# Optimization experiments

Hardware: AMD Instinct MI355X
Metric: run time of the kernel (lower is better)

## Reference

```python
import jax, jax.numpy as jnp
import numpy as np

N = 50000
E = 800000
IN_C = 256
OUT_C = 128
HID = 2 * OUT_C  # 256


def setup_inputs() -> dict:
    key = jax.random.key(0)
    ks = jax.random.split(key, 8)
    def glorot(k, fan_in, fan_out):
        lim = (6.0 / (fan_in + fan_out)) ** 0.5
        return jax.random.uniform(k, (fan_in, fan_out), jnp.float32, -lim, lim)
    x = jax.random.normal(ks[0], (N, IN_C), dtype=jnp.float32)
    edge_index = jax.random.randint(ks[1], (2, E), 0, N, dtype=jnp.int64)
    return {
        "x": x,
        "edge_index": edge_index,
        "W1": glorot(ks[2], IN_C, HID),
        "b1": jnp.zeros((HID,), jnp.float32),
        "W_mu": glorot(ks[3], HID, OUT_C),
        "b_mu": jnp.zeros((OUT_C,), jnp.float32),
        "W_ls": glorot(ks[4], HID, OUT_C),
        "b_ls": jnp.zeros((OUT_C,), jnp.float32),
    }


def _gcn_norm(edge_index, n):
    # PyG GCNConv default: add self-loops, symmetric normalization D^-1/2 A D^-1/2
    loop = jnp.arange(n, dtype=edge_index.dtype)
    src = jnp.concatenate([edge_index[0], loop])  # [E+N]
    dst = jnp.concatenate([edge_index[1], loop])
    deg = jax.ops.segment_sum(jnp.ones_like(dst, dtype=jnp.float32), dst, num_segments=n)
    dinv = jnp.where(deg > 0, jax.lax.rsqrt(deg), 0.0)
    norm = dinv[src] * dinv[dst]  # [E+N]
    return src, dst, norm


def _gcn_conv(x, W, b, src, dst, norm, n):
    h = x @ W                                   # [N, F_out] transform first (F_out < F_in ok)
    msg = h[src] * norm[:, None]                # [E+N, F_out] gather + scale
    out = jax.ops.segment_sum(msg, dst, num_segments=n)  # scatter-add aggregate
    return out + b


def reference(x, edge_index, W1, b1, W_mu, b_mu, W_ls, b_ls):
    n = x.shape[0]
    src, dst, norm = _gcn_norm(edge_index, n)
    h = jax.nn.relu(_gcn_conv(x, W1, b1, src, dst, norm, n))
    mu = _gcn_conv(h, W_mu, b_mu, src, dst, norm, n)
    logstd = _gcn_conv(h, W_ls, b_ls, src, dst, norm, n)
    return (mu, logstd)
```

## Files before the change

### kernel.cpp

```cpp
#include <hip/hip_runtime.h>

#define NN 50000
#define EE 800000
#define NBIN 391
#define BINCAP 2560
#define NB_P1 391
#define NB_PB 256

typedef _Float16 half8 __attribute__((ext_vector_type(8)));
typedef float f32x4 __attribute__((ext_vector_type(4)));
typedef unsigned short ushort8v __attribute__((ext_vector_type(8)));
typedef unsigned short ushort4v __attribute__((ext_vector_type(4)));

__device__ __forceinline__ unsigned short f2h(float f){
  _Float16 h = (_Float16)f; unsigned short u; __builtin_memcpy(&u, &h, 2); return u;
}
__device__ __forceinline__ float h2f(unsigned short u){
  _Float16 h; __builtin_memcpy(&h, &u, 2); return (float)h;
}
__device__ __forceinline__ void split2h(float v, unsigned short* p){
  _Float16 hi = (_Float16)v;
  _Float16 lo = (_Float16)(v - (float)hi);
  __builtin_memcpy(p, &hi, 2);
  __builtin_memcpy(p+1, &lo, 2);
}
__device__ __forceinline__ void gl2lds16(const unsigned short* g, unsigned short* l){
  __builtin_amdgcn_global_load_lds(
    (const __attribute__((address_space(1))) unsigned int*)g,
    (__attribute__((address_space(3))) unsigned int*)l, 16, 0, 0);
}

__device__ __forceinline__ int detect_m(const int* eidx, int* sh){
  int t = threadIdx.x;
  if (t < 64){
    int v = eidx[2*t + 1];
    unsigned long long nz = __ballot(v != 0);
    if (t == 0) *sh = (nz == 0ULL) ? 1 : 0;
  }
  __syncthreads();
  return *sh;
}

__global__ __launch_bounds__(512) void k_prep(const int* __restrict__ eidx,
    const float* __restrict__ W1,
    const float* __restrict__ Wmu, const float* __restrict__ Wls,
    int* __restrict__ gcur, unsigned int* __restrict__ binbuf,
    unsigned short* __restrict__ Bt1, unsigned short* __restrict__ Bt2){
  int b = blockIdx.x;
  int tid = threadIdx.x;
  if (b < NB_P1){
    __shared__ int msh;
    __shared__ int hist[NBIN];
    __shared__ int base[NBIN];
    int m = detect_m(eidx, &msh);
    for (int k = tid; k < NBIN; k += 512) hist[k] = 0;
    __syncthreads();
    int sv[4], dl[4], cb[4], ofs[4];
    #pragma unroll
    for (int j = 0; j < 4; ++j){
      int e = b*2048 + j*512 + tid;
      cb[j] = -1;
      if (e < EE){
        sv[j] = m ? eidx[2*e]        : eidx[e];
        int d  = m ? eidx[2*(EE + e)] : eidx[EE + e];
        cb[j] = d >> 7; dl[j] = d & 127;
        ofs[j] = atomicAdd(&hist[cb[j]], 1);
      }
    }
    __syncthreads();
    for (int k = tid; k < NBIN; k += 512)
      base[k] = hist[k] ? atomicAdd(&gcur[k], hist[k]) : 0;
    __syncthreads();
    #pragma unroll
    for (int j = 0; j < 4; ++j){
      if (cb[j] >= 0){
        int p = base[cb[j]] + ofs[j];
        if (p < BINCAP)
          binbuf[(size_t)cb[j]*BINCAP + p] = (unsigned)sv[j] | ((unsigned)dl[j] << 16);
      }
    }
  } else {
    int gid = (b - NB_P1)*512 + tid;
    int idx = gid & 65535;
    int n = idx & 255, k = idx >> 8;
    if (gid < 65536){
      unsigned short hq = f2h(W1[k*256 + n]);
      unsigned short* p = Bt1 + (size_t)n*512 + 2*k;
      p[0] = hq; p[1] = hq;
    } else {
      float w = (n < 128) ? Wmu[k*128 + n] : Wls[k*128 + (n - 128)];
      Bt2[(size_t)n*256 + k] = f2h(w);
    }
  }
}

__global__ __launch_bounds__(512) void k_pass2(const unsigned int* __restrict__ binbuf,
    const int* __restrict__ gcur, int* __restrict__ cnt,
    unsigned short* __restrict__ bk){
  __shared__ int lcnt[128];
  __shared__ __align__(16) unsigned short lbk[128*64];
  int c = blockIdx.x;
  int tid = threadIdx.x;
  if (tid < 128) lcnt[tid] = 0;
  __syncthreads();
  int n = gcur[c]; if (n > BINCAP) n = BINCAP;
  const unsigned int* bb = binbuf + (size_t)c*BINCAP;
  for (int t = tid; t < n; t += 512){
    unsigned v = bb[t];
    int dloc = v >> 16;
    int slot = atomicAdd(&lcnt[dloc], 1);
    if (slot < 64) lbk[dloc*64 + slot] = (unsigned short)(v & 0xFFFF);
  }
  __syncthreads();
  #pragma unroll
  for (int k = 0; k < 2; ++k){
    int idx = k*512 + tid;
    int node = c*128 + (idx >> 3);
    if (node < NN)
      *(uint4*)(bk + (size_t)c*128*64 + idx*8) = *(const uint4*)(lbk + idx*8);
  }
  if (tid < 128){
    int node = c*128 + tid;
    if (node < NN) cnt[node] = lcnt[tid];
  }
}

__global__ __launch_bounds__(256) void k_gemm8x(const float* __restrict__ X,
    const unsigned short* __restrict__ Bt, unsigned short* __restrict__ C,
    int M, const int* __restrict__ cnt){
  __shared__ __align__(16) unsigned short sA[128*64];
  __shared__ __align__(16) unsigned short sB[128*64];
  const int g = blockIdx.x;
  const int xc = g & 7, s = g >> 3;
  const int tN = s & 1;
  const int tM = (s >> 1)*8 + xc;
  const int nTM = (M + 127) >> 7;
  if (tM >= nTM) return;
  const int tid  = threadIdx.x;
  const int wave = tid >> 6, lane = tid & 63;
  const int wm = wave >> 1, wn = wave & 1;
  const int quad = lane >> 4, l16 = lane & 15;
  const int rsub = lane >> 3;
  const int l7   = lane & 7;
  const int chs  = l7 ^ rsub;

  f32x4 acc[4][4] = {};

  for (int kt = 0; kt < 8; ++kt){
    #pragma unroll
    for (int j = 0; j < 4; ++j){
      int q = wave*4 + j;
      int r = q*8 + rsub;
      gl2lds16(Bt + (size_t)(tN*128 + r)*512 + kt*64 + chs*8, &sB[q*512]);
    }
    float4 v[4];
    #pragma unroll
    for (int j = 0; j < 4; ++j){
      int q = wave*4 + j;
      int r = q*8 + rsub;
      int arow = tM*128 + r; if (arow >= M) arow = M-1;
      v[j] = *(const float4*)(X + (size_t)arow*256 + kt*32 + chs*4);
    }
    #pragma unroll
    for (int j = 0; j < 4; ++j){
      int q = wave*4 + j;
      __attribute__((aligned(16))) unsigned short sh[8];
      split2h(v[j].x, sh); split2h(v[j].y, sh+2);
      split2h(v[j].z, sh+4); split2h(v[j].w, sh+6);
      *(uint4*)(&sA[q*512 + (rsub*8 + l7)*8]) = *(const uint4*)(sh);
    }
    __syncthreads();
    #pragma unroll
    for (int ks = 0; ks < 2; ++ks){
      half8 af[4], bfr[4];
      #pragma unroll
      for (int t = 0; t < 4; ++t){
        int R = wm*64 + t*16 + l16;
        af[t]  = *(const half8*)(&sA[R*64 + ((ks*4 + quad) ^ (R & 7))*8]);
      }
      #pragma unroll
      for (int t = 0; t < 4; ++t){
        int R = wn*64 + t*16 + l16;
        bfr[t] = *(const half8*)(&sB[R*64 + ((ks*4 + quad) ^ (R & 7))*8]);
      }
      #pragma unroll
      for (int mt = 0; mt < 4; ++mt)
        #pragma unroll
        for (int nt = 0; nt < 4; ++nt)
          acc[mt][nt] = __builtin_amdgcn_mfma_f32_16x16x32_f16(af[mt], bfr[nt], acc[mt][nt], 0, 0, 0);
    }
    __syncthreads();
  }

  #pragma unroll
  for (int mt = 0; mt < 4; ++mt){
    #pragma unroll
    for (int r = 0; r < 4; ++r){
      int row = tM*128 + wm*64 + mt*16 + quad*4 + r;
      if (row < M){
        float sc = rsqrtf((float)(cnt[row] + 1));
        #pragma unroll
        for (int nt = 0; nt < 4; ++nt){
          int cc = tN*128 + wn*64 + nt*16 + l16;
          C[(size_t)row*256 + cc] = f2h(acc[mt][nt][r] * sc);
        }
      }
    }
  }
}

template<int KT, int SCALE>
__global__ __launch_bounds__(256) void k_gemm(const unsigned short* __restrict__ Asp,
                                              const unsigned short* __restrict__ Bt,
                                              unsigned short* __restrict__ C, int M,
                                              const int* __restrict__ cnt){
  __shared__ __align__(16) unsigned short sA[128*64];
  __shared__ __align__(16) unsigned short sB[128*64];
  const int g = blockIdx.x;
  const int xc = g & 7, s = g >> 3;
  const int tN = s & 1;
  const int tM = (s >> 1)*8 + xc;
  const int nTM = (M + 127) >> 7;
  if (tM >= nTM) return;
  const int tid  = threadIdx.x;
  const int wave = tid >> 6, lane = tid & 63;
  const int wm = wave >> 1, wn = wave & 1;
  const int quad = lane >> 4, l16 = lane & 15;
  const int rsub = lane >> 3;
  const int chs  = (lane & 7) ^ rsub;

  f32x4 acc[4][4] = {};

  for (int kt = 0; kt < KT; ++kt){
    #pragma unroll
    for (int j = 0; j < 4; ++j){
      int q = wave*4 + j;
      int r = q*8 + rsub;
      int arow = tM*128 + r; if (arow >= M) arow = M-1;
      gl2lds16(Asp + (size_t)arow*(KT*64) + kt*64 + chs*8, &sA[q*512]);
      gl2lds16(Bt  + (size_t)(tN*128 + r)*(KT*64) + kt*64 + chs*8, &sB[q*512]);
    }
    __syncthreads();
    #pragma unroll
    for (int ks = 0; ks < 2; ++ks){
      half8 af[4], bfr[4];
      #pragma unroll
      for (int t = 0; t < 4; ++t){
        int R = wm*64 + t*16 + l16;
        af[t]  = *(const half8*)(&sA[R*64 + ((ks*4 + quad) ^ (R & 7))*8]);
      }
      #pragma unroll
      for (int t = 0; t < 4; ++t){
        int R = wn*64 + t*16 + l16;
        bfr[t] = *(const half8*)(&sB[R*64 + ((ks*4 + quad) ^ (R & 7))*8]);
      }
      #pragma unroll
      for (int mt = 0; mt < 4; ++mt)
        #pragma unroll
        for (int nt = 0; nt < 4; ++nt)
          acc[mt][nt] = __builtin_amdgcn_mfma_f32_16x16x32_f16(af[mt], bfr[nt], acc[mt][nt], 0, 0, 0);
    }
    __syncthreads();
  }

  #pragma unroll
  for (int mt = 0; mt < 4; ++mt){
    #pragma unroll
    for (int r = 0; r < 4; ++r){
      int row = tM*128 + wm*64 + mt*16 + quad*4 + r;
      if (row < M){
        float sc = 1.f;
        if (SCALE) sc = rsqrtf((float)(cnt[row] + 1));
        #pragma unroll
        for (int nt = 0; nt < 4; ++nt){
          int cc = tN*128 + wn*64 + nt*16 + l16;
          C[(size_t)row*256 + cc] = f2h(acc[mt][nt][r] * sc);
        }
      }
    }
  }
}

__global__ __launch_bounds__(256) void k_agg_relu(const unsigned short* __restrict__ feat,
    const int* __restrict__ cnt, const unsigned short* __restrict__ bkall,
    const float* __restrict__ b1, unsigned short* __restrict__ h1){
  int i = blockIdx.x*4 + (threadIdx.x >> 6);
  int lane = threadIdx.x & 63;
  int f0 = lane*4;
  int deg = cnt[i]; if (deg > 64) deg = 64;
  float di = rsqrtf((float)(deg + 1));
  const unsigned short* bk = bkall + ((size_t)i << 6);
  ushort4 hv = *(const ushort4*)(feat + (size_t)i*256 + f0);
  float p0 = h2f(hv.x), p1 = h2f(hv.y), p2 = h2f(hv.z), p3 = h2f(hv.w);
  float q0=0.f,q1=0.f,q2=0.f,q3=0.f, r0=0.f,r1=0.f,r2=0.f,r3=0.f, t0=0.f,t1=0.f,t2=0.f,t3=0.f;
  int e = 0;
  for (; e + 8 <= deg; e += 8){
    ushort8v sa = *(const ushort8v*)(bk + e);
    ushort4 v0 = *(const ushort4*)(feat + (size_t)sa[0]*256 + f0);
    ushort4 v1 = *(const ushort4*)(feat + (size_t)sa[1]*256 + f0);
    ushort4 v2 = *(const ushort4*)(feat + (size_t)sa[2]*256 + f0);
    ushort4 v3 = *(const ushort4*)(feat + (size_t)sa[3]*256 + f0);
    ushort4 v4 = *(const ushort4*)(feat + (size_t)sa[4]*256 + f0);
    ushort4 v5 = *(const ushort4*)(feat + (size_t)sa[5]*256 + f0);
    ushort4 v6 = *(const ushort4*)(feat + (size_t)sa[6]*256 + f0);
    ushort4 v7 = *(const ushort4*)(feat + (size_t)sa[7]*256 + f0);
    p0 += h2f(v0.x); p1 += h2f(v0.y); p2 += h2f(v0.z); p3 += h2f(v0.w);
    q0 += h2f(v1.x); q1 += h2f(v1.y); q2 += h2f(v1.z); q3 += h2f(v1.w);
    r0 += h2f(v2.x); r1 += h2f(v2.y); r2 += h2f(v2.z); r3 += h2f(v2.w);
    t0 += h2f(v3.x); t1 += h2f(v3.y); t2 += h2f(v3.z); t3 += h2f(v3.w);
    p0 += h2f(v4.x); p1 += h2f(v4.y); p2 += h2f(v4.z); p3 += h2f(v4.w);
    q0 += h2f(v5.x); q1 += h2f(v5.y); q2 += h2f(v5.z); q3 += h2f(v5.w);
    r0 += h2f(v6.x); r1 += h2f(v6.y); r2 += h2f(v6.z); r3 += h2f(v6.w);
    t0 += h2f(v7.x); t1 += h2f(v7.y); t2 += h2f(v7.z); t3 += h2f(v7.w);
  }
  if (e + 4 <= deg){
    ushort4v sa = *(const ushort4v*)(bk + e);
    ushort4 v0 = *(const ushort4*)(feat + (size_t)sa[0]*256 + f0);
    ushort4 v1 = *(const ushort4*)(feat + (size_t)sa[1]*256 + f0);
    ushort4 v2 = *(const ushort4*)(feat + (size_t)sa[2]*256 + f0);
    ushort4 v3 = *(const ushort4*)(feat + (size_t)sa[3]*256 + f0);
    p0 += h2f(v0.x); p1 += h2f(v0.y); p2 += h2f(v0.z); p3 += h2f(v0.w);
    q0 += h2f(v1.x); q1 += h2f(v1.y); q2 += h2f(v1.z); q3 += h2f(v1.w);
    r0 += h2f(v2.x); r1 += h2f(v2.y); r2 += h2f(v2.z); r3 += h2f(v2.w);
    t0 += h2f(v3.x); t1 += h2f(v3.y); t2 += h2f(v3.z); t3 += h2f(v3.w);
    e += 4;
  }
  for (; e < deg; ++e){
    int s = bk[e];
    ushort4 v = *(const ushort4*)(feat + (size_t)s*256 + f0);
    p0 += h2f(v.x); p1 += h2f(v.y); p2 += h2f(v.z); p3 += h2f(v.w);
  }
  float s0 = p0+q0+r0+t0, s1 = p1+q1+r1+t1, s2 = p2+q2+r2+t2, s3 = p3+q3+r3+t3;
  float4 bb = *(const float4*)(b1 + f0);
  float u0 = fmaxf(di*s0 + bb.x, 0.f);
  float u1 = fmaxf(di*s1 + bb.y, 0.f);
  float u2 = fmaxf(di*s2 + bb.z, 0.f);
  float u3 = fmaxf(di*s3 + bb.w, 0.f);
  ushort4 o;
  o.x = f2h(di*u0); o.y = f2h(di*u1); o.z = f2h(di*u2); o.w = f2h(di*u3);
  *(ushort4*)(h1 + (size_t)i*256 + f0) = o;
}

__global__ __launch_bounds__(256) void k_agg_out(const unsigned short* __restrict__ feat,
    const int* __restrict__ cnt, const unsigned short* __restrict__ bkall,
    const float* __restrict__ bmu, const float* __restrict__ bls, float* __restrict__ outp){
  int i = blockIdx.x*4 + (threadIdx.x >> 6);
  int lane = threadIdx.x & 63;
  int f0 = lane*4;
  int deg = cnt[i]; if (deg > 64) deg = 64;
  float di = rsqrtf((float)(deg + 1));
  const unsigned short* bk = bkall + ((size_t)i << 6);
  ushort4 hv = *(const ushort4*)(feat + (size_t)i*256 + f0);
  float p0 = h2f(hv.x), p1 = h2f(hv.y), p2 = h2f(hv.z), p3 = h2f(hv.w);
  float q0=0.f,q1=0.f,q2=0.f,q3=0.f, r0=0.f,r1=0.f,r2=0.f,r3=0.f, t0=0.f,t1=0.f,t2=0.f,t3=0.f;
  int e = 0;
  for (; e + 8 <= deg; e += 8){
    ushort8v sa = *(const ushort8v*)(bk + e);
    ushort4 v0 = *(const ushort4*)(feat + (size_t)sa[0]*256 + f0);
    ushort4 v1 = *(const ushort4*)(feat + (size_t)sa[1]*256 + f0);
    ushort4 v2 = *(const ushort4*)(feat + (size_t)sa[2]*256 + f0);
    ushort4 v3 = *(const ushort4*)(feat + (size_t)sa[3]*256 + f0);
    ushort4 v4 = *(const ushort4*)(feat + (size_t)sa[4]*256 + f0);
    ushort4 v5 = *(const ushort4*)(feat + (size_t)sa[5]*256 + f0);
    ushort4 v6 = *(const ushort4*)(feat + (size_t)sa[6]*256 + f0);
    ushort4 v7 = *(const ushort4*)(feat + (size_t)sa[7]*256 + f0);
    p0 += h2f(v0.x); p1 += h2f(v0.y); p2 += h2f(v0.z); p3 += h2f(v0.w);
    q0 += h2f(v1.x); q1 += h2f(v1.y); q2 += h2f(v1.z); q3 += h2f(v1.w);
    r0 += h2f(v2.x); r1 += h2f(v2.y); r2 += h2f(v2.z); r3 += h2f(v2.w);
    t0 += h2f(v3.x); t1 += h2f(v3.y); t2 += h2f(v3.z); t3 += h2f(v3.w);
    p0 += h2f(v4.x); p1 += h2f(v4.y); p2 += h2f(v4.z); p3 += h2f(v4.w);
    q0 += h2f(v5.x); q1 += h2f(v5.y); q2 += h2f(v5.z); q3 += h2f(v5.w);
    r0 += h2f(v6.x); r1 += h2f(v6.y); r2 += h2f(v6.z); r3 += h2f(v6.w);
    t0 += h2f(v7.x); t1 += h2f(v7.y); t2 += h2f(v7.z); t3 += h2f(v7.w);
  }
  if (e + 4 <= deg){
    ushort4v sa = *(const ushort4v*)(bk + e);
    ushort4 v0 = *(const ushort4*)(feat + (size_t)sa[0]*256 + f0);
    ushort4 v1 = *(const ushort4*)(feat + (size_t)sa[1]*256 + f0);
    ushort4 v2 = *(const ushort4*)(feat + (size_t)sa[2]*256 + f0);
    ushort4 v3 = *(const ushort4*)(feat + (size_t)sa[3]*256 + f0);
    p0 += h2f(v0.x); p1 += h2f(v0.y); p2 += h2f(v0.z); p3 += h2f(v0.w);
    q0 += h2f(v1.x); q1 += h2f(v1.y); q2 += h2f(v1.z); q3 += h2f(v1.w);
    r0 += h2f(v2.x); r1 += h2f(v2.y); r2 += h2f(v2.z); r3 += h2f(v2.w);
    t0 += h2f(v3.x); t1 += h2f(v3.y); t2 += h2f(v3.z); t3 += h2f(v3.w);
    e += 4;
  }
  for (; e < deg; ++e){
    int s = bk[e];
    ushort4 v = *(const ushort4*)(feat + (size_t)s*256 + f0);
    p0 += h2f(v.x); p1 += h2f(v.y); p2 += h2f(v.z); p3 += h2f(v.w);
  }
  float a0 = di*(p0+q0+r0+t0), a1 = di*(p1+q1+r1+t1);
  float a2 = di*(p2+q2+r2+t2), a3 = di*(p3+q3+r3+t3);
  float4 o;
  if (f0 < 128){
    float4 bb = *(const float4*)(bmu + f0);
    o.x = a0 + bb.x; o.y = a1 + bb.y; o.z = a2 + bb.z; o.w = a3 + bb.w;
    *(float4*)(outp + (size_t)i*128 + f0) = o;
  } else {
    int g = f0 - 128;
    float4 bb = *(const float4*)(bls + g);
    o.x = a0 + bb.x; o.y = a1 + bb.y; o.z = a2 + bb.z; o.w = a3 + bb.w;
    *(float4*)(outp + (size_t)NN*128 + (size_t)i*128 + g) = o;
  }
}

extern "C" void kernel_launch(void* const* d_in, const int* in_sizes, int n_in,
                              void* d_out, int out_size, void* d_ws, size_t ws_size,
                              hipStream_t stream){
  const float* x   = (const float*)d_in[0];
  const int* eidx  = (const int*)d_in[1];
  const float* W1  = (const float*)d_in[2];
  const float* b1  = (const float*)d_in[3];
  const float* Wmu = (const float*)d_in[4];
  const float* bmu = (const float*)d_in[5];
  const float* Wls = (const float*)d_in[6];
  const float* bls = (const float*)d_in[7];
  float* out = (float*)d_out;

  char* ws = (char*)d_ws;
  size_t off = 0;
  auto alloc = [&](size_t bytes)->char*{
    char* p = ws + off; off = (off + bytes + 511) & ~(size_t)511; return p;
  };
  int* gcur     = (int*)alloc(NBIN*4);
  unsigned int* binbuf = (unsigned int*)alloc((size_t)NBIN*BINCAP*4);
  int* cnt      = (int*)alloc(NN*4);
  unsigned short* buckets = (unsigned short*)alloc((size_t)NN*64*2);
  unsigned short* Bt1 = (unsigned short*)alloc((size_t)256*512*2);
  unsigned short* Bt2 = (unsigned short*)alloc((size_t)256*256*2);
  unsigned short* h1  = (unsigned short*)alloc((size_t)NN*256*2);
  unsigned short* h   = (unsigned short*)alloc((size_t)NN*256*2);
  unsigned short* z   = h;

  hipMemsetAsync(gcur, 0, NBIN*4, stream);
  k_prep<<<NB_P1 + NB_PB, 512, 0, stream>>>(eidx, W1, Wmu, Wls,
                                            gcur, binbuf, Bt1, Bt2);
  k_pass2<<<NBIN, 512, 0, stream>>>(binbuf, gcur, cnt, buckets);
  k_gemm8x<<<784, 256, 0, stream>>>(x, Bt1, h, NN, cnt);
  k_agg_relu<<<12500, 256, 0, stream>>>(h, cnt, buckets, b1, h1);
  k_gemm<4,0><<<784, 256, 0, stream>>>(h1, Bt2, z, NN, cnt);
  k_agg_out<<<12500, 256, 0, stream>>>(z, cnt, buckets, bmu, bls, out);
}
```

Before: 294.8 us.

## Software-pipeline both GEMM kernels with double-buffered B tiles and register-prefetched A

Both GEMM kernels now double-buffer the B tile in LDS and prefetch the next A slice into registers while the current K-step's MFMAs run, using explicit waitcnt and s_barrier in place of __syncthreads. The second GEMM loads A through registers instead of direct global-to-LDS copies, and its unused scale path is dropped. Launch bounds request 3 blocks per CU. The aim is to hide global load latency behind compute, at the cost of more LDS and registers per block, which could limit occupancy.

```diff
diff --git a/kernel.cpp b/kernel.cpp
--- a/kernel.cpp
+++ b/kernel.cpp
@@ -125,11 +125,11 @@
   }
 }
 
-__global__ __launch_bounds__(256) void k_gemm8x(const float* __restrict__ X,
+__global__ __launch_bounds__(256, 3) void k_gemm8x(const float* __restrict__ X,
     const unsigned short* __restrict__ Bt, unsigned short* __restrict__ C,
     int M, const int* __restrict__ cnt){
   __shared__ __align__(16) unsigned short sA[128*64];
-  __shared__ __align__(16) unsigned short sB[128*64];
+  __shared__ __align__(16) unsigned short sB[2][128*64];
   const int g = blockIdx.x;
   const int xc = g & 7, s = g >> 3;
   const int tN = s & 1;
@@ -144,32 +144,53 @@
   const int l7   = lane & 7;
   const int chs  = l7 ^ rsub;
 
+  int arow[4];
+  #pragma unroll
+  for (int j = 0; j < 4; ++j){
+    int q = wave*4 + j, r = q*8 + rsub;
+    int a = tM*128 + r; if (a >= M) a = M-1;
+    arow[j] = a;
+  }
+
   f32x4 acc[4][4] = {};
 
+  #pragma unroll
+  for (int j = 0; j < 4; ++j){
+    int q = wave*4 + j, r = q*8 + rsub;
+    gl2lds16(Bt + (size_t)(tN*128 + r)*512 + chs*8, &sB[0][q*512]);
+  }
+  __builtin_amdgcn_sched_barrier(0);
+  float4 v[4];
+  float4 vn[4] = {};
+  #pragma unroll
+  for (int j = 0; j < 4; ++j)
+    v[j] = *(const float4*)(X + (size_t)arow[j]*256 + chs*4);
+
+  #pragma unroll
   for (int kt = 0; kt < 8; ++kt){
-    #pragma unroll
-    for (int j = 0; j < 4; ++j){
-      int q = wave*4 + j;
-      int r = q*8 + rsub;
-      gl2lds16(Bt + (size_t)(tN*128 + r)*512 + kt*64 + chs*8, &sB[q*512]);
-    }
-    float4 v[4];
-    #pragma unroll
-    for (int j = 0; j < 4; ++j){
-      int q = wave*4 + j;
-      int r = q*8 + rsub;
-      int arow = tM*128 + r; if (arow >= M) arow = M-1;
-      v[j] = *(const float4*)(X + (size_t)arow*256 + kt*32 + chs*4);
-    }
     #pragma unroll
     for (int j = 0; j < 4; ++j){
       int q = wave*4 + j;
       __attribute__((aligned(16))) unsigned short sh[8];
-      split2h(v[j].x, sh); split2h(v[j].y, sh+2);
+      split2h(v[j].x, sh);   split2h(v[j].y, sh+2);
       split2h(v[j].z, sh+4); split2h(v[j].w, sh+6);
-      *(uint4*)(&sA[q*512 + (rsub*8 + l7)*8]) = *(const uint4*)(sh);
-    }
-    __syncthreads();
+      *(uint4*)(&sA[q*512 + lane*8]) = *(const uint4*)(sh);
+    }
+    if (kt < 7){
+      #pragma unroll
+      for (int j = 0; j < 4; ++j){
+        int q = wave*4 + j, r = q*8 + rsub;
+        gl2lds16(Bt + (size_t)(tN*128 + r)*512 + (kt+1)*64 + chs*8,
+                 &sB[(kt+1)&1][q*512]);
+      }
+      __builtin_amdgcn_sched_barrier(0);
+      #pragma unroll
+      for (int j = 0; j < 4; ++j)
+        vn[j] = *(const float4*)(X + (size_t)arow[j]*256 + (kt+1)*32 + chs*4);
+    }
+    asm volatile("s_waitcnt lgkmcnt(0)" ::: "memory");
+    __builtin_amdgcn_sched_barrier(0);
+    __builtin_amdgcn_s_barrier();
     #pragma unroll
     for (int ks = 0; ks < 2; ++ks){
       half8 af[4], bfr[4];
@@ -181,7 +202,7 @@
       #pragma unroll
       for (int t = 0; t < 4; ++t){
         int R = wn*64 + t*16 + l16;
-        bfr[t] = *(const half8*)(&sB[R*64 + ((ks*4 + quad) ^ (R & 7))*8]);
+        bfr[t] = *(const half8*)(&sB[kt & 1][R*64 + ((ks*4 + quad) ^ (R & 7))*8]);
       }
       #pragma unroll
       for (int mt = 0; mt < 4; ++mt)
@@ -189,7 +210,11 @@
         for (int nt = 0; nt < 4; ++nt)
           acc[mt][nt] = __builtin_amdgcn_mfma_f32_16x16x32_f16(af[mt], bfr[nt], acc[mt][nt], 0, 0, 0);
     }
-    __syncthreads();
+    asm volatile("s_waitcnt lgkmcnt(0)" ::: "memory");
+    __builtin_amdgcn_sched_barrier(0);
+    __builtin_amdgcn_s_barrier();
+    #pragma unroll
+    for (int j = 0; j < 4; ++j) v[j] = vn[j];
   }
 
   #pragma unroll
@@ -209,13 +234,10 @@
   }
 }
 
-template<int KT, int SCALE>
-__global__ __launch_bounds__(256) void k_gemm(const unsigned short* __restrict__ Asp,
-                                              const unsigned short* __restrict__ Bt,
-                                              unsigned short* __restrict__ C, int M,
-                                              const int* __restrict__ cnt){
+__global__ __launch_bounds__(256, 3) void k_gemm4p(const unsigned short* __restrict__ A,
+    const unsigned short* __restrict__ Bt, unsigned short* __restrict__ C, int M){
   __shared__ __align__(16) unsigned short sA[128*64];
-  __shared__ __align__(16) unsigned short sB[128*64];
+  __shared__ __align__(16) unsigned short sB[2][128*64];
   const int g = blockIdx.x;
   const int xc = g & 7, s = g >> 3;
   const int tN = s & 1;
@@ -227,20 +249,53 @@
   const int wm = wave >> 1, wn = wave & 1;
   const int quad = lane >> 4, l16 = lane & 15;
   const int rsub = lane >> 3;
-  const int chs  = (lane & 7) ^ rsub;
+  const int l7   = lane & 7;
+  const int chs  = l7 ^ rsub;
+
+  int arow[4];
+  #pragma unroll
+  for (int j = 0; j < 4; ++j){
+    int q = wave*4 + j, r = q*8 + rsub;
+    int a = tM*128 + r; if (a >= M) a = M-1;
+    arow[j] = a;
+  }
 
   f32x4 acc[4][4] = {};
 
-  for (int kt = 0; kt < KT; ++kt){
+  #pragma unroll
+  for (int j = 0; j < 4; ++j){
+    int q = wave*4 + j, r = q*8 + rsub;
+    gl2lds16(Bt + (size_t)(tN*128 + r)*256 + chs*8, &sB[0][q*512]);
+  }
+  __builtin_amdgcn_sched_barrier(0);
+  uint4 av[4];
+  uint4 avn[4] = {};
+  #pragma unroll
+  for (int j = 0; j < 4; ++j)
+    av[j] = *(const uint4*)(A + (size_t)arow[j]*256 + chs*8);
+
+  #pragma unroll
+  for (int kt = 0; kt < 4; ++kt){
     #pragma unroll
     for (int j = 0; j < 4; ++j){
       int q = wave*4 + j;
-      int r = q*8 + rsub;
-      int arow = tM*128 + r; if (arow >= M) arow = M-1;
-      gl2lds16(Asp + (size_t)arow*(KT*64) + kt*64 + chs*8, &sA[q*512]);
-      gl2lds16(Bt  + (size_t)(tN*128 + r)*(KT*64) + kt*64 + chs*8, &sB[q*512]);
-    }
-    __syncthreads();
+      *(uint4*)(&sA[q*512 + lane*8]) = av[j];
+    }
+    if (kt < 3){
+      #pragma unroll
+      for (int j = 0; j < 4; ++j){
+        int q = wave*4 + j, r = q*8 + rsub;
+        gl2lds16(Bt + (size_t)(tN*128 + r)*256 + (kt+1)*64 + chs*8,
+                 &sB[(kt+1)&1][q*512]);
+      }
+      __builtin_amdgcn_sched_barrier(0);
+      #pragma unroll
+      for (int j = 0; j < 4; ++j)
+        avn[j] = *(const uint4*)(A + (size_t)arow[j]*256 + (kt+1)*64 + chs*8);
+    }
+    asm volatile("s_waitcnt lgkmcnt(0)" ::: "memory");
+    __builtin_amdgcn_sched_barrier(0);
+    __builtin_amdgcn_s_barrier();
     #pragma unroll
     for (int ks = 0; ks < 2; ++ks){
       half8 af[4], bfr[4];
@@ -252,7 +307,7 @@
       #pragma unroll
       for (int t = 0; t < 4; ++t){
         int R = wn*64 + t*16 + l16;
-        bfr[t] = *(const half8*)(&sB[R*64 + ((ks*4 + quad) ^ (R & 7))*8]);
+        bfr[t] = *(const half8*)(&sB[kt & 1][R*64 + ((ks*4 + quad) ^ (R & 7))*8]);
       }
       #pragma unroll
       for (int mt = 0; mt < 4; ++mt)
@@ -260,7 +315,11 @@
         for (int nt = 0; nt < 4; ++nt)
           acc[mt][nt] = __builtin_amdgcn_mfma_f32_16x16x32_f16(af[mt], bfr[nt], acc[mt][nt], 0, 0, 0);
     }
-    __syncthreads();
+    asm volatile("s_waitcnt lgkmcnt(0)" ::: "memory");
+    __builtin_amdgcn_sched_barrier(0);
+    __builtin_amdgcn_s_barrier();
+    #pragma unroll
+    for (int j = 0; j < 4; ++j) av[j] = avn[j];
   }
 
   #pragma unroll
@@ -269,12 +328,10 @@
     for (int r = 0; r < 4; ++r){
       int row = tM*128 + wm*64 + mt*16 + quad*4 + r;
       if (row < M){
-        float sc = 1.f;
-        if (SCALE) sc = rsqrtf((float)(cnt[row] + 1));
         #pragma unroll
         for (int nt = 0; nt < 4; ++nt){
           int cc = tN*128 + wn*64 + nt*16 + l16;
-          C[(size_t)row*256 + cc] = f2h(acc[mt][nt][r] * sc);
+          C[(size_t)row*256 + cc] = f2h(acc[mt][nt][r]);
         }
       }
     }
@@ -439,6 +496,6 @@
   k_pass2<<<NBIN, 512, 0, stream>>>(binbuf, gcur, cnt, buckets);
   k_gemm8x<<<784, 256, 0, stream>>>(x, Bt1, h, NN, cnt);
   k_agg_relu<<<12500, 256, 0, stream>>>(h, cnt, buckets, b1, h1);
-  k_gemm<4,0><<<784, 256, 0, stream>>>(h1, Bt2, z, NN, cnt);
+  k_gemm4p<<<784, 256, 0, stream>>>(h1, Bt2, z, NN);
   k_agg_out<<<12500, 256, 0, stream>>>(z, cnt, buckets, bmu, bls, out);
 }
```

After: 291.2 us. Within noise of the previous version (-1.2%).
